# Kernel optimization log

Measured on AMD Instinct MI355X. Metric: run time of the kernel, lower is better.

## Reference

```python
import jax, jax.numpy as jnp
import numpy as np

N, D_I, D_O = 512, 128, 128


def _xavier(key, shape):
    fan_out, fan_in = shape
    limit = np.sqrt(6.0 / (fan_in + fan_out))
    return jax.random.uniform(key, shape, jnp.float32, -limit, limit)


def setup_inputs() -> dict:
    key = jax.random.key(0)
    k1, k2, k3, k4 = jax.random.split(key, 4)
    x = jax.random.normal(k1, (N, D_I), jnp.float32)
    adj = jax.random.randint(k2, (N, N), 0, 2, jnp.int32)
    Wf = _xavier(k3, (D_O, 2 * D_I))   # nn.Linear(2*d_i, d_o).weight
    bf = jnp.zeros((D_O,), jnp.float32)
    Ww = _xavier(k4, (1, 2 * D_I))     # nn.Linear(2*d_i, 1).weight
    bw = jnp.zeros((1,), jnp.float32)
    return {"x": x, "adj": adj, "Wf": Wf, "bf": bf, "Ww": Ww, "bw": bw}


def reference(x, adj, Wf, bf, Ww, bw):
    # h[i, j] = concat(x[j], x[i])  (hsrc varies along j, htgt along i)
    # score a[i, j] = Ww . h[i, j] + bw  -> split Ww into src/tgt halves
    w_src, w_tgt = Ww[0, :D_I], Ww[0, D_I:]
    a = x @ w_src + (x @ w_tgt)[:, None] + bw[0]          # [N, N]
    a_msk = jnp.where(adj > 0, a, jnp.float32(-1e16))
    a_att = jax.nn.softmax(a_msk, axis=1)                  # softmax over j

    # message y[i, j] = relu(Wf . h[i, j] + bf)
    f_src = x @ Wf[:, :D_I].T                              # [N, d_o] (j part)
    f_tgt = x @ Wf[:, D_I:].T                              # [N, d_o] (i part)
    y = jax.nn.relu(f_src[None, :, :] + f_tgt[:, None, :] + bf)  # [N, N, d_o]

    o = jnp.einsum('ij,ijd->id', a_att, y)                 # weighted sum over j
    return (o, a_att)
```

## Files before the change

### kernel.cpp

```cpp
#include <hip/hip_runtime.h>
#include <math.h>

#define N   512
#define DI  128
#define DO  128


__global__ __launch_bounds__(256) void wt_kernel(
    const float* __restrict__ Wf, float* __restrict__ WT)
{
    const int k = blockIdx.x;
    const int c = threadIdx.x;
    WT[k * 256 + c] = Wf[(c & 127) * 256 + (c >> 7) * 128 + k];
}

__global__ __launch_bounds__(256) void proj_kernel(
    const float* __restrict__ x,
    const float* __restrict__ WT,
    const float* __restrict__ Ww,
    float* __restrict__ fsrc,
    float* __restrict__ ftgt,
    float* __restrict__ s,
    float* __restrict__ t)
{
    const int jb = blockIdx.x * 2;
    const int c  = threadIdx.x;

    const float* __restrict__ x0 = x + jb * DI;
    const float* __restrict__ x1 = x0 + DI;

    float acc0 = 0.f, acc1 = 0.f;
#pragma unroll 16
    for (int k = 0; k < DI; ++k) {
        const float wv = WT[k * 256 + c];
        acc0 += x0[k] * wv;
        acc1 += x1[k] * wv;
    }
    if (c < DO) {
        fsrc[(jb + 0) * DO + c] = acc0;
        fsrc[(jb + 1) * DO + c] = acc1;
    } else {
        ftgt[(jb + 0) * DO + (c - DO)] = acc0;
        ftgt[(jb + 1) * DO + (c - DO)] = acc1;
    }

    const int w = c >> 6;
    const int l = c & 63;
    const int row = jb + (w >> 1);
    const int half = (w & 1) * DI;
    const float* __restrict__ xr = x + row * DI;
    float v = xr[l] * Ww[half + l] + xr[64 + l] * Ww[half + 64 + l];
    for (int off = 32; off >= 1; off >>= 1)
        v += __shfl_down(v, off);
    if (l == 0) {
        if ((w & 1) == 0) s[row] = v;
        else              t[row] = v;
    }
}

__global__ __launch_bounds__(512) void gat_kernel(
    const int*   __restrict__ adj,
    const float* __restrict__ fsrc,
    const float* __restrict__ ftgt,
    const float* __restrict__ s,
    const float* __restrict__ t,
    const float* __restrict__ bf,
    const float* __restrict__ bw,
    float* __restrict__ out)
{
    const int i0  = blockIdx.x * 2;
    const int tid = threadIdx.x;

    __shared__ float p[N][2];
    __shared__ float red[16][2][DO];
    __shared__ float rmax[2][4];
    __shared__ float rsum[2][4];

    const int r  = tid >> 8;
    const int jj = tid & 255;
    const int i  = i0 + r;
    const float t_i = t[i] + bw[0];

    const float sc0 = s[jj] + t_i;
    const float sc1 = s[jj + 256] + t_i;
    const float v0 = (adj[i * N + jj] > 0)       ? sc0 : -1e16f;
    const float v1 = (adj[i * N + jj + 256] > 0) ? sc1 : -1e16f;

    const int wr = (tid >> 6) & 3;
    float m = fmaxf(v0, v1);
    for (int off = 32; off >= 1; off >>= 1)
        m = fmaxf(m, __shfl_down(m, off));
    if ((tid & 63) == 0) rmax[r][wr] = m;
    __syncthreads();
    m = fmaxf(fmaxf(rmax[r][0], rmax[r][1]), fmaxf(rmax[r][2], rmax[r][3]));

    const float e0 = __expf(v0 - m);
    const float e1 = __expf(v1 - m);
    float sum = e0 + e1;
    for (int off = 32; off >= 1; off >>= 1)
        sum += __shfl_down(sum, off);
    if ((tid & 63) == 0) rsum[r][wr] = sum;
    __syncthreads();
    sum = rsum[r][0] + rsum[r][1] + rsum[r][2] + rsum[r][3];
    const float inv = 1.0f / sum;

    const float p0 = e0 * inv;
    const float p1 = e1 * inv;
    p[jj][r]       = p0;
    p[jj + 256][r] = p1;
    out[N * DO + i * N + jj]       = p0;
    out[N * DO + i * N + jj + 256] = p1;
    __syncthreads();

    const int c4 = (tid & 31) * 4;
    const int jg = tid >> 5;

    const float4 fA = *(const float4*)&ftgt[i0 * DO + c4];
    const float4 fB = *(const float4*)&ftgt[(i0 + 1) * DO + c4];
    const float4 bb = *(const float4*)&bf[c4];
    const float ftbAx = fA.x + bb.x, ftbAy = fA.y + bb.y,
                ftbAz = fA.z + bb.z, ftbAw = fA.w + bb.w;
    const float ftbBx = fB.x + bb.x, ftbBy = fB.y + bb.y,
                ftbBz = fB.z + bb.z, ftbBw = fB.w + bb.w;

    float ax = 0.f, ay = 0.f, az = 0.f, aw = 0.f;
    float bx = 0.f, by = 0.f, bz = 0.f, bw_ = 0.f;

    const int jstart = jg * 32;
#pragma unroll 8
    for (int j = jstart; j < jstart + 32; ++j) {
        const float4 f = *(const float4*)&fsrc[j * DO + c4];
        const float2 pv = *(const float2*)&p[j][0];
        const float yx = fmaxf(f.x + ftbAx, 0.f);
        const float yy = fmaxf(f.y + ftbAy, 0.f);
        const float yz = fmaxf(f.z + ftbAz, 0.f);
        const float yw = fmaxf(f.w + ftbAw, 0.f);
        ax += pv.x * yx; ay += pv.x * yy; az += pv.x * yz; aw += pv.x * yw;
        const float zx = fmaxf(f.x + ftbBx, 0.f);
        const float zy = fmaxf(f.y + ftbBy, 0.f);
        const float zz = fmaxf(f.z + ftbBz, 0.f);
        const float zw = fmaxf(f.w + ftbBw, 0.f);
        bx += pv.y * zx; by += pv.y * zy; bz += pv.y * zz; bw_ += pv.y * zw;
    }

    *(float4*)&red[jg][0][c4] = make_float4(ax, ay, az, aw);
    *(float4*)&red[jg][1][c4] = make_float4(bx, by, bz, bw_);
    __syncthreads();

    if (tid < 256) {
        const int rr = tid >> 7;
        const int cc = tid & 127;
        float acc = 0.f;
#pragma unroll
        for (int g = 0; g < 16; ++g)
            acc += red[g][rr][cc];
        out[(i0 + rr) * DO + cc] = acc;
    }
}

extern "C" void kernel_launch(void* const* d_in, const int* in_sizes, int n_in,
                              void* d_out, int out_size, void* d_ws, size_t ws_size,
                              hipStream_t stream) {
    const float* x   = (const float*)d_in[0];
    const int*   adj = (const int*)  d_in[1];
    const float* Wf  = (const float*)d_in[2];
    const float* bf  = (const float*)d_in[3];
    const float* Ww  = (const float*)d_in[4];
    const float* bw  = (const float*)d_in[5];
    float* out = (float*)d_out;

    float* WT   = (float*)d_ws;
    float* fsrc = WT + 128 * 256;
    float* ftgt = fsrc + N * DO;
    float* s    = ftgt + N * DO;
    float* t    = s + N;

    wt_kernel  <<<dim3(128), dim3(256), 0, stream>>>(Wf, WT);
    proj_kernel<<<dim3(256), dim3(256), 0, stream>>>(x, WT, Ww, fsrc, ftgt, s, t);
    gat_kernel <<<dim3(256), dim3(512), 0, stream>>>(adj, fsrc, ftgt, s, t, bf, bw, out);
}
```

Before: 21.56 us.

## Fuse three kernels into one cooperative kernel with grid-wide syncs

Merges the weight-transpose, projection and attention kernels into a single cooperative launch, separated by grid.sync barriers, so two kernel launch gaps go away. The projection is also restructured to use 512 threads that split K into four slices, read float4 weights and reduce the partial sums in shared memory. The cost is two grid-wide barriers and a larger shared-memory footprint per block. Cooperative launch also requires all 256 blocks to be resident at once.

```diff
diff --git a/kernel.cpp b/kernel.cpp
--- a/kernel.cpp
+++ b/kernel.cpp
@@ -1,160 +1,172 @@
 #include <hip/hip_runtime.h>
+#include <hip/hip_cooperative_groups.h>
 #include <math.h>
+
+namespace cg = cooperative_groups;
 
 #define N   512
 #define DI  128
 #define DO  128
 
-
-__global__ __launch_bounds__(256) void wt_kernel(
-    const float* __restrict__ Wf, float* __restrict__ WT)
-{
-    const int k = blockIdx.x;
-    const int c = threadIdx.x;
-    WT[k * 256 + c] = Wf[(c & 127) * 256 + (c >> 7) * 128 + k];
-}
-
-__global__ __launch_bounds__(256) void proj_kernel(
+__global__ __launch_bounds__(512) void gat_fused_kernel(
     const float* __restrict__ x,
-    const float* __restrict__ WT,
+    const int*   __restrict__ adj,
+    const float* __restrict__ Wf,
+    const float* __restrict__ bf,
     const float* __restrict__ Ww,
+    const float* __restrict__ bw,
+    float* __restrict__ out,
+    float* __restrict__ WT,
     float* __restrict__ fsrc,
     float* __restrict__ ftgt,
     float* __restrict__ s,
     float* __restrict__ t)
 {
-    const int jb = blockIdx.x * 2;
-    const int c  = threadIdx.x;
-
-    const float* __restrict__ x0 = x + jb * DI;
-    const float* __restrict__ x1 = x0 + DI;
-
-    float acc0 = 0.f, acc1 = 0.f;
-#pragma unroll 16
-    for (int k = 0; k < DI; ++k) {
-        const float wv = WT[k * 256 + c];
-        acc0 += x0[k] * wv;
-        acc1 += x1[k] * wv;
-    }
-    if (c < DO) {
-        fsrc[(jb + 0) * DO + c] = acc0;
-        fsrc[(jb + 1) * DO + c] = acc1;
-    } else {
-        ftgt[(jb + 0) * DO + (c - DO)] = acc0;
-        ftgt[(jb + 1) * DO + (c - DO)] = acc1;
-    }
-
-    const int w = c >> 6;
-    const int l = c & 63;
-    const int row = jb + (w >> 1);
-    const int half = (w & 1) * DI;
-    const float* __restrict__ xr = x + row * DI;
-    float v = xr[l] * Ww[half + l] + xr[64 + l] * Ww[half + 64 + l];
-    for (int off = 32; off >= 1; off >>= 1)
-        v += __shfl_down(v, off);
-    if (l == 0) {
-        if ((w & 1) == 0) s[row] = v;
-        else              t[row] = v;
-    }
-}
-
-__global__ __launch_bounds__(512) void gat_kernel(
-    const int*   __restrict__ adj,
-    const float* __restrict__ fsrc,
-    const float* __restrict__ ftgt,
-    const float* __restrict__ s,
-    const float* __restrict__ t,
-    const float* __restrict__ bf,
-    const float* __restrict__ bw,
-    float* __restrict__ out)
-{
-    const int i0  = blockIdx.x * 2;
+    cg::grid_group grid = cg::this_grid();
+    const int b   = blockIdx.x;
     const int tid = threadIdx.x;
 
+    __shared__ float accbuf[2][4][256];
     __shared__ float p[N][2];
     __shared__ float red[16][2][DO];
-    __shared__ float rmax[2][4];
-    __shared__ float rsum[2][4];
+    __shared__ float rmax[2][4], rsum[2][4];
 
-    const int r  = tid >> 8;
-    const int jj = tid & 255;
-    const int i  = i0 + r;
-    const float t_i = t[i] + bw[0];
+    if (b < 64) {
+        const int e = b * 512 + tid;
+        const int k = e >> 8, c = e & 255;
+        WT[e] = Wf[(c & 127) * 256 + (c >> 7) * 128 + k];
+    }
+    grid.sync();
 
-    const float sc0 = s[jj] + t_i;
-    const float sc1 = s[jj + 256] + t_i;
-    const float v0 = (adj[i * N + jj] > 0)       ? sc0 : -1e16f;
-    const float v1 = (adj[i * N + jj + 256] > 0) ? sc1 : -1e16f;
+    const int j0 = b * 2;
+    {
+        const int r   = tid >> 8;
+        const int ks  = (tid >> 6) & 3;
+        const int cg4 = (tid & 63) * 4;
+        const float* __restrict__ xr = x + (j0 + r) * DI + ks * 32;
 
-    const int wr = (tid >> 6) & 3;
-    float m = fmaxf(v0, v1);
-    for (int off = 32; off >= 1; off >>= 1)
-        m = fmaxf(m, __shfl_down(m, off));
-    if ((tid & 63) == 0) rmax[r][wr] = m;
-    __syncthreads();
-    m = fmaxf(fmaxf(rmax[r][0], rmax[r][1]), fmaxf(rmax[r][2], rmax[r][3]));
+        float ax = 0.f, ay = 0.f, az = 0.f, aw = 0.f;
+#pragma unroll
+        for (int kk = 0; kk < 32; ++kk) {
+            const float4 w4 = *(const float4*)&WT[(ks * 32 + kk) * 256 + cg4];
+            const float  xv = xr[kk];
+            ax += xv * w4.x; ay += xv * w4.y; az += xv * w4.z; aw += xv * w4.w;
+        }
+        *(float4*)&accbuf[r][ks][cg4] = make_float4(ax, ay, az, aw);
 
-    const float e0 = __expf(v0 - m);
-    const float e1 = __expf(v1 - m);
-    float sum = e0 + e1;
-    for (int off = 32; off >= 1; off >>= 1)
-        sum += __shfl_down(sum, off);
-    if ((tid & 63) == 0) rsum[r][wr] = sum;
-    __syncthreads();
-    sum = rsum[r][0] + rsum[r][1] + rsum[r][2] + rsum[r][3];
-    const float inv = 1.0f / sum;
+        const int w = tid >> 6;
+        if (w < 4) {
+            const int row  = j0 + (w >> 1);
+            const int half = (w & 1) * DI;
+            const int l    = tid & 63;
+            float v = x[row * DI + l] * Ww[half + l]
+                    + x[row * DI + 64 + l] * Ww[half + 64 + l];
+            for (int off = 32; off >= 1; off >>= 1)
+                v += __shfl_down(v, off);
+            if (l == 0) {
+                if ((w & 1) == 0) s[row] = v;
+                else              t[row] = v;
+            }
+        }
+        __syncthreads();
 
-    const float p0 = e0 * inv;
-    const float p1 = e1 * inv;
-    p[jj][r]       = p0;
-    p[jj + 256][r] = p1;
-    out[N * DO + i * N + jj]       = p0;
-    out[N * DO + i * N + jj + 256] = p1;
-    __syncthreads();
+        if (tid < 128) {
+            const int r2 = tid >> 6;
+            const int cg = tid & 63;
+            const float4 a0 = *(const float4*)&accbuf[r2][0][cg * 4];
+            const float4 a1 = *(const float4*)&accbuf[r2][1][cg * 4];
+            const float4 a2 = *(const float4*)&accbuf[r2][2][cg * 4];
+            const float4 a3 = *(const float4*)&accbuf[r2][3][cg * 4];
+            const float4 sm = make_float4(a0.x + a1.x + a2.x + a3.x,
+                                          a0.y + a1.y + a2.y + a3.y,
+                                          a0.z + a1.z + a2.z + a3.z,
+                                          a0.w + a1.w + a2.w + a3.w);
+            if (cg < 32) *(float4*)&fsrc[(j0 + r2) * DO + cg * 4] = sm;
+            else         *(float4*)&ftgt[(j0 + r2) * DO + (cg - 32) * 4] = sm;
+        }
+    }
+    grid.sync();
 
-    const int c4 = (tid & 31) * 4;
-    const int jg = tid >> 5;
+    const int i0 = j0;
+    {
+        const int r  = tid >> 8;
+        const int jj = tid & 255;
+        const int i  = i0 + r;
+        const float t_i = t[i] + bw[0];
 
-    const float4 fA = *(const float4*)&ftgt[i0 * DO + c4];
-    const float4 fB = *(const float4*)&ftgt[(i0 + 1) * DO + c4];
-    const float4 bb = *(const float4*)&bf[c4];
-    const float ftbAx = fA.x + bb.x, ftbAy = fA.y + bb.y,
-                ftbAz = fA.z + bb.z, ftbAw = fA.w + bb.w;
-    const float ftbBx = fB.x + bb.x, ftbBy = fB.y + bb.y,
-                ftbBz = fB.z + bb.z, ftbBw = fB.w + bb.w;
+        const float sc0 = s[jj] + t_i;
+        const float sc1 = s[jj + 256] + t_i;
+        const float v0 = (adj[i * N + jj] > 0)       ? sc0 : -1e16f;
+        const float v1 = (adj[i * N + jj + 256] > 0) ? sc1 : -1e16f;
 
-    float ax = 0.f, ay = 0.f, az = 0.f, aw = 0.f;
-    float bx = 0.f, by = 0.f, bz = 0.f, bw_ = 0.f;
+        const int wr = (tid >> 6) & 3;
+        float m = fmaxf(v0, v1);
+        for (int off = 32; off >= 1; off >>= 1)
+            m = fmaxf(m, __shfl_down(m, off));
+        if ((tid & 63) == 0) rmax[r][wr] = m;
+        __syncthreads();
+        m = fmaxf(fmaxf(rmax[r][0], rmax[r][1]), fmaxf(rmax[r][2], rmax[r][3]));
 
-    const int jstart = jg * 32;
+        const float e0 = __expf(v0 - m);
+        const float e1 = __expf(v1 - m);
+        float sum = e0 + e1;
+        for (int off = 32; off >= 1; off >>= 1)
+            sum += __shfl_down(sum, off);
+        if ((tid & 63) == 0) rsum[r][wr] = sum;
+        __syncthreads();
+        sum = rsum[r][0] + rsum[r][1] + rsum[r][2] + rsum[r][3];
+        const float inv = 1.0f / sum;
+
+        const float p0 = e0 * inv;
+        const float p1 = e1 * inv;
+        p[jj][r]       = p0;
+        p[jj + 256][r] = p1;
+        out[N * DO + i * N + jj]       = p0;
+        out[N * DO + i * N + jj + 256] = p1;
+        __syncthreads();
+
+        const int c4 = (tid & 31) * 4;
+        const int jg = tid >> 5;
+
+        const float4 fA = *(const float4*)&ftgt[i0 * DO + c4];
+        const float4 fB = *(const float4*)&ftgt[(i0 + 1) * DO + c4];
+        const float4 bb = *(const float4*)&bf[c4];
+        const float ftbAx = fA.x + bb.x, ftbAy = fA.y + bb.y,
+                    ftbAz = fA.z + bb.z, ftbAw = fA.w + bb.w;
+        const float ftbBx = fB.x + bb.x, ftbBy = fB.y + bb.y,
+                    ftbBz = fB.z + bb.z, ftbBw = fB.w + bb.w;
+
+        float ax = 0.f, ay = 0.f, az = 0.f, aw = 0.f;
+        float bx = 0.f, by = 0.f, bz = 0.f, bw_ = 0.f;
+
+        const int jstart = jg * 32;
 #pragma unroll 8
-    for (int j = jstart; j < jstart + 32; ++j) {
-        const float4 f = *(const float4*)&fsrc[j * DO + c4];
-        const float2 pv = *(const float2*)&p[j][0];
-        const float yx = fmaxf(f.x + ftbAx, 0.f);
-        const float yy = fmaxf(f.y + ftbAy, 0.f);
-        const float yz = fmaxf(f.z + ftbAz, 0.f);
-        const float yw = fmaxf(f.w + ftbAw, 0.f);
-        ax += pv.x * yx; ay += pv.x * yy; az += pv.x * yz; aw += pv.x * yw;
-        const float zx = fmaxf(f.x + ftbBx, 0.f);
-        const float zy = fmaxf(f.y + ftbBy, 0.f);
-        const float zz = fmaxf(f.z + ftbBz, 0.f);
-        const float zw = fmaxf(f.w + ftbBw, 0.f);
-        bx += pv.y * zx; by += pv.y * zy; bz += pv.y * zz; bw_ += pv.y * zw;
-    }
+        for (int j = jstart; j < jstart + 32; ++j) {
+            const float4 f = *(const float4*)&fsrc[j * DO + c4];
+            const float2 pv = *(const float2*)&p[j][0];
+            ax += pv.x * fmaxf(f.x + ftbAx, 0.f);
+            ay += pv.x * fmaxf(f.y + ftbAy, 0.f);
+            az += pv.x * fmaxf(f.z + ftbAz, 0.f);
+            aw += pv.x * fmaxf(f.w + ftbAw, 0.f);
+            bx += pv.y * fmaxf(f.x + ftbBx, 0.f);
+            by += pv.y * fmaxf(f.y + ftbBy, 0.f);
+            bz += pv.y * fmaxf(f.z + ftbBz, 0.f);
+            bw_ += pv.y * fmaxf(f.w + ftbBw, 0.f);
+        }
 
-    *(float4*)&red[jg][0][c4] = make_float4(ax, ay, az, aw);
-    *(float4*)&red[jg][1][c4] = make_float4(bx, by, bz, bw_);
-    __syncthreads();
+        *(float4*)&red[jg][0][c4] = make_float4(ax, ay, az, aw);
+        *(float4*)&red[jg][1][c4] = make_float4(bx, by, bz, bw_);
+        __syncthreads();
 
-    if (tid < 256) {
-        const int rr = tid >> 7;
-        const int cc = tid & 127;
-        float acc = 0.f;
+        if (tid < 256) {
+            const int rr = tid >> 7;
+            const int cc = tid & 127;
+            float acc = 0.f;
 #pragma unroll
-        for (int g = 0; g < 16; ++g)
-            acc += red[g][rr][cc];
-        out[(i0 + rr) * DO + cc] = acc;
+            for (int g = 0; g < 16; ++g)
+                acc += red[g][rr][cc];
+            out[(i0 + rr) * DO + cc] = acc;
+        }
     }
 }
 
@@ -175,7 +187,10 @@
     float* s    = ftgt + N * DO;
     float* t    = s + N;
 
-    wt_kernel  <<<dim3(128), dim3(256), 0, stream>>>(Wf, WT);
-    proj_kernel<<<dim3(256), dim3(256), 0, stream>>>(x, WT, Ww, fsrc, ftgt, s, t);
-    gat_kernel <<<dim3(256), dim3(512), 0, stream>>>(adj, fsrc, ftgt, s, t, bf, bw, out);
+    void* args[] = {
+        (void*)&x, (void*)&adj, (void*)&Wf, (void*)&bf, (void*)&Ww, (void*)&bw,
+        (void*)&out, (void*)&WT, (void*)&fsrc, (void*)&ftgt, (void*)&s, (void*)&t
+    };
+    hipLaunchCooperativeKernel((void*)gat_fused_kernel,
+                               dim3(256), dim3(512), args, 0, stream);
 }
```

New measurement: 80.10 us. 271% more time.
